# Performance work log

Measured on AMD Instinct MI355X. Metric: run time of the kernel, lower is better.

Reference implementation:

```python
import jax, jax.numpy as jnp
import numpy as np

STRIDE = 1
PADDING = 1


def setup_inputs() -> dict:
    key = jax.random.key(0)
    k1, k2, k3 = jax.random.split(key, 3)
    x = jax.random.normal(k1, (16, 64, 224, 224), dtype=jnp.float32)
    W = jax.random.normal(k2, (64, 64, 3, 3), dtype=jnp.float32)
    b = jax.random.normal(k3, (64,), dtype=jnp.float32)
    return {"x": x, "W": W, "b": b}


def reference(x, W, b):
    # Equivalent of the naive im2col+GEMM conv: a standard 2D convolution
    # (cross-correlation) with stride/padding, NCHW layout, OIHW weights.
    out = jax.lax.conv_general_dilated(
        x, W,
        window_strides=(STRIDE, STRIDE),
        padding=[(PADDING, PADDING), (PADDING, PADDING)],
        dimension_numbers=("NCHW", "OIHW", "NCHW"),
    )
    return out + b[None, :, None, None]
```

## Files before the change

kernel.cpp:

```cpp
#include <hip/hip_runtime.h>
#include <hip/hip_bf16.h>


typedef __attribute__((ext_vector_type(8)))  short   short8;
typedef __attribute__((ext_vector_type(8)))  unsigned short ushort8;
typedef __attribute__((ext_vector_type(16))) float   float16_t;

#define HW (224 * 224)

__device__ __forceinline__ unsigned short f2bf(float f) {
  __hip_bfloat16 h = __float2bfloat16(f);
  return *reinterpret_cast<unsigned short*>(&h);
}

__global__ void build_wt(const float* __restrict__ W, unsigned short* __restrict__ wt) {
  int i = blockIdx.x * 256 + threadIdx.x;
  if (i < 9 * 64 * 64) {
    int tap = i >> 12;
    int rem = i & 4095;
    int nn  = rem >> 6;
    int c   = rem & 63;
    wt[i] = f2bf(W[(nn * 64 + c) * 9 + tap]);
  }
}

__global__ __launch_bounds__(256, 2) void conv3x3_mfma(
    const float* __restrict__ x, const unsigned short* __restrict__ wt,
    const float* __restrict__ bias, float* __restrict__ out) {
  __shared__ __align__(16) unsigned short xs[18 * 8 * 34 * 8];

  const int w0  = blockIdx.x * 32;
  const int h0  = blockIdx.y * 16;
  const int img = blockIdx.z;
  const int tid = threadIdx.x;
  const int lane = tid & 63, wave = tid >> 6;
  const int ln31 = lane & 31, lhi = lane >> 5;

  const float* xn = x + (size_t)img * 64 * HW;

  for (int i = tid; i < 18 * 8 * 34; i += 256) {
    int h   = i / (8 * 34);
    int rem = i - h * (8 * 34);
    int cg  = rem / 34;
    int w   = rem - cg * 34;
    int gh = h0 - 1 + h;
    int gw = w0 - 1 + w;
    ushort8 pk;
    if ((unsigned)gh < 224u && (unsigned)gw < 224u) {
      const float* p = xn + (size_t)cg * 8 * HW + gh * 224 + gw;
#pragma unroll
      for (int j = 0; j < 8; ++j) pk[j] = f2bf(p[(size_t)j * HW]);
    } else {
#pragma unroll
      for (int j = 0; j < 8; ++j) pk[j] = 0;
    }
    *reinterpret_cast<ushort8*>(&xs[i * 8]) = pk;
  }
  __syncthreads();

  const int row0 = wave * 4;
  float16_t acc[4][2];
#pragma unroll
  for (int rb = 0; rb < 4; ++rb)
#pragma unroll
    for (int nb = 0; nb < 2; ++nb) acc[rb][nb] = 0.f;

#pragma unroll
  for (int r = 0; r < 3; ++r) {
#pragma unroll
    for (int s = 0; s < 3; ++s) {
      const int tap = r * 3 + s;
      short8 bq[4][2];
#pragma unroll
      for (int ks = 0; ks < 4; ++ks)
#pragma unroll
        for (int nb = 0; nb < 2; ++nb)
          bq[ks][nb] = *reinterpret_cast<const short8*>(
              wt + ((tap * 64 + nb * 32 + ln31) * 64 + ks * 16 + lhi * 8));

#pragma unroll
      for (int ks = 0; ks < 4; ++ks) {
        const int cg = ks * 2 + lhi;
#pragma unroll
        for (int rb = 0; rb < 4; ++rb) {
          const int hidx = row0 + rb + r;
          const int widx = ln31 + s;
          const short8 a = *reinterpret_cast<const short8*>(
              &xs[(((hidx * 8) + cg) * 34 + widx) * 8]);
          acc[rb][0] = __builtin_amdgcn_mfma_f32_32x32x16_bf16(a, bq[ks][0], acc[rb][0], 0, 0, 0);
          acc[rb][1] = __builtin_amdgcn_mfma_f32_32x32x16_bf16(a, bq[ks][1], acc[rb][1], 0, 0, 0);
        }
      }
    }
  }

#pragma unroll
  for (int rb = 0; rb < 4; ++rb) {
    const int h = h0 + row0 + rb;
#pragma unroll
    for (int nb = 0; nb < 2; ++nb) {
      const int ch = nb * 32 + ln31;
      const float bv = bias[ch];
      float* op = out + (((size_t)img * 64 + ch) * 224 + h) * 224 + w0;
#pragma unroll
      for (int q = 0; q < 4; ++q) {
        const int wloc = 8 * q + 4 * lhi;
        float4 v;
        v.x = acc[rb][nb][4 * q + 0] + bv;
        v.y = acc[rb][nb][4 * q + 1] + bv;
        v.z = acc[rb][nb][4 * q + 2] + bv;
        v.w = acc[rb][nb][4 * q + 3] + bv;
        *reinterpret_cast<float4*>(op + wloc) = v;
      }
    }
  }
}

#define TW 32
#define TH 32
#define KB 16
#define PXT 4
__global__ __launch_bounds__(256) void conv3x3_direct(
    const float* __restrict__ x, const float* __restrict__ wgt,
    const float* __restrict__ bias, float* __restrict__ out) {
  __shared__ float xsf[34 * 35];
  const int tx = blockIdx.x % 7, ty = blockIdx.x / 7;
  const int k0 = blockIdx.y * KB, n = blockIdx.z;
  const int w0 = tx * TW, h0 = ty * TH;
  const int tid = threadIdx.x;
  const int tw = tid & 7, th = tid >> 3;
  float acc[KB][PXT];
#pragma unroll
  for (int k = 0; k < KB; ++k)
#pragma unroll
    for (int p = 0; p < PXT; ++p) acc[k][p] = 0.f;
  const float* xn = x + (size_t)n * 64 * HW;
  for (int c = 0; c < 64; ++c) {
    const float* xc = xn + (size_t)c * HW;
    for (int i = tid; i < 34 * 34; i += 256) {
      int row = i / 34, col = i - row * 34;
      int gh = h0 - 1 + row, gw = w0 - 1 + col;
      float v = 0.f;
      if (gh >= 0 && gh < 224 && gw >= 0 && gw < 224) v = xc[gh * 224 + gw];
      xsf[row * 35 + col] = v;
    }
    __syncthreads();
    float in[3][6];
#pragma unroll
    for (int r = 0; r < 3; ++r)
#pragma unroll
      for (int q = 0; q < 6; ++q) in[r][q] = xsf[(th + r) * 35 + tw * PXT + q];
    const float* wc = wgt + ((size_t)k0 * 64 + c) * 9;
#pragma unroll
    for (int k = 0; k < KB; ++k) {
      const float* wk = wc + (size_t)k * 64 * 9;
#pragma unroll
      for (int r = 0; r < 3; ++r)
#pragma unroll
        for (int s = 0; s < 3; ++s) {
          float wv = wk[r * 3 + s];
#pragma unroll
          for (int p = 0; p < PXT; ++p) acc[k][p] += wv * in[r][s + p];
        }
    }
    __syncthreads();
  }
#pragma unroll
  for (int k = 0; k < KB; ++k) {
    float bv = bias[k0 + k];
    float4 v = make_float4(acc[k][0] + bv, acc[k][1] + bv, acc[k][2] + bv, acc[k][3] + bv);
    float* op = out + ((((size_t)n * 64 + (k0 + k)) * 224 + (h0 + th)) * 224 + (w0 + tw * PXT));
    *reinterpret_cast<float4*>(op) = v;
  }
}

extern "C" void kernel_launch(void* const* d_in, const int* in_sizes, int n_in,
                              void* d_out, int out_size, void* d_ws, size_t ws_size,
                              hipStream_t stream) {
  const float* x = (const float*)d_in[0];
  const float* W = (const float*)d_in[1];
  const float* b = (const float*)d_in[2];
  float* out = (float*)d_out;

  if (ws_size >= 9 * 64 * 64 * sizeof(unsigned short)) {
    unsigned short* wt = (unsigned short*)d_ws;
    build_wt<<<144, 256, 0, stream>>>(W, wt);
    dim3 grid(7, 14, 16);
    conv3x3_mfma<<<grid, 256, 0, stream>>>(x, wt, b, out);
  } else {
    dim3 grid(7 * 7, 64 / KB, 16);
    conv3x3_direct<<<grid, 256, 0, stream>>>(x, W, b, out);
  }
}
```

Baseline: 469.8 us.

## Use 512-thread blocks with two rows per wave and swapped MFMA operands

The MFMA conv kernel now runs 512 threads (8 waves) per block, each wave computing 2 output rows instead of 4. Register pressure drops because it keeps half the accumulators and loads the weight fragments per k-step instead of holding all of them. The MFMA A/B operands are swapped so each lane holds output channels along the accumulator and width along lanes. The epilogue therefore writes scalar stores coalesced across width instead of float4 stores. The aim is higher occupancy and latency hiding, at the cost of more weight reloads per wave and scalar instead of vector stores.

```diff
diff --git a/kernel.cpp b/kernel.cpp
--- a/kernel.cpp
+++ b/kernel.cpp
@@ -24,7 +24,7 @@
   }
 }
 
-__global__ __launch_bounds__(256, 2) void conv3x3_mfma(
+__global__ __launch_bounds__(512, 4) void conv3x3_mfma(
     const float* __restrict__ x, const unsigned short* __restrict__ wt,
     const float* __restrict__ bias, float* __restrict__ out) {
   __shared__ __align__(16) unsigned short xs[18 * 8 * 34 * 8];
@@ -38,7 +38,7 @@
 
   const float* xn = x + (size_t)img * 64 * HW;
 
-  for (int i = tid; i < 18 * 8 * 34; i += 256) {
+  for (int i = tid; i < 18 * 8 * 34; i += 512) {
     int h   = i / (8 * 34);
     int rem = i - h * (8 * 34);
     int cg  = rem / 34;
@@ -58,10 +58,10 @@
   }
   __syncthreads();
 
-  const int row0 = wave * 4;
-  float16_t acc[4][2];
+  const int row0 = wave * 2;
+  float16_t acc[2][2];
 #pragma unroll
-  for (int rb = 0; rb < 4; ++rb)
+  for (int rb = 0; rb < 2; ++rb)
 #pragma unroll
     for (int nb = 0; nb < 2; ++nb) acc[rb][nb] = 0.f;
 
@@ -70,47 +70,40 @@
 #pragma unroll
     for (int s = 0; s < 3; ++s) {
       const int tap = r * 3 + s;
-      short8 bq[4][2];
-#pragma unroll
-      for (int ks = 0; ks < 4; ++ks)
-#pragma unroll
-        for (int nb = 0; nb < 2; ++nb)
-          bq[ks][nb] = *reinterpret_cast<const short8*>(
-              wt + ((tap * 64 + nb * 32 + ln31) * 64 + ks * 16 + lhi * 8));
-
 #pragma unroll
       for (int ks = 0; ks < 4; ++ks) {
+        const short8 b0 = *reinterpret_cast<const short8*>(
+            wt + ((tap * 64 + 0 * 32 + ln31) * 64 + ks * 16 + lhi * 8));
+        const short8 b1 = *reinterpret_cast<const short8*>(
+            wt + ((tap * 64 + 1 * 32 + ln31) * 64 + ks * 16 + lhi * 8));
         const int cg = ks * 2 + lhi;
 #pragma unroll
-        for (int rb = 0; rb < 4; ++rb) {
+        for (int rb = 0; rb < 2; ++rb) {
           const int hidx = row0 + rb + r;
           const int widx = ln31 + s;
           const short8 a = *reinterpret_cast<const short8*>(
               &xs[(((hidx * 8) + cg) * 34 + widx) * 8]);
-          acc[rb][0] = __builtin_amdgcn_mfma_f32_32x32x16_bf16(a, bq[ks][0], acc[rb][0], 0, 0, 0);
-          acc[rb][1] = __builtin_amdgcn_mfma_f32_32x32x16_bf16(a, bq[ks][1], acc[rb][1], 0, 0, 0);
+          acc[rb][0] = __builtin_amdgcn_mfma_f32_32x32x16_bf16(b0, a, acc[rb][0], 0, 0, 0);
+          acc[rb][1] = __builtin_amdgcn_mfma_f32_32x32x16_bf16(b1, a, acc[rb][1], 0, 0, 0);
         }
       }
     }
   }
 
 #pragma unroll
-  for (int rb = 0; rb < 4; ++rb) {
+  for (int rb = 0; rb < 2; ++rb) {
     const int h = h0 + row0 + rb;
 #pragma unroll
     for (int nb = 0; nb < 2; ++nb) {
-      const int ch = nb * 32 + ln31;
-      const float bv = bias[ch];
-      float* op = out + (((size_t)img * 64 + ch) * 224 + h) * 224 + w0;
 #pragma unroll
       for (int q = 0; q < 4; ++q) {
-        const int wloc = 8 * q + 4 * lhi;
-        float4 v;
-        v.x = acc[rb][nb][4 * q + 0] + bv;
-        v.y = acc[rb][nb][4 * q + 1] + bv;
-        v.z = acc[rb][nb][4 * q + 2] + bv;
-        v.w = acc[rb][nb][4 * q + 3] + bv;
-        *reinterpret_cast<float4*>(op + wloc) = v;
+#pragma unroll
+        for (int j = 0; j < 4; ++j) {
+          const int m  = j + 8 * q + 4 * lhi;
+          const int ch = nb * 32 + m;
+          const float v = acc[rb][nb][4 * q + j] + bias[ch];
+          out[(((size_t)img * 64 + ch) * 224 + h) * 224 + w0 + ln31] = v;
+        }
       }
     }
   }
@@ -186,7 +179,7 @@
     unsigned short* wt = (unsigned short*)d_ws;
     build_wt<<<144, 256, 0, stream>>>(W, wt);
     dim3 grid(7, 14, 16);
-    conv3x3_mfma<<<grid, 256, 0, stream>>>(x, wt, b, out);
+    conv3x3_mfma<<<grid, 512, 0, stream>>>(x, wt, b, out);
   } else {
     dim3 grid(7 * 7, 64 / KB, 16);
     conv3x3_direct<<<grid, 256, 0, stream>>>(x, W, b, out);
```

Result: slower. 506.0 us (+7.7%).
